# Kernel tuning notes

Hardware: AMD Instinct MI355X
Metric: run time of the kernel (lower is better)

The kernel has to match this reference:

```python
import jax, jax.numpy as jnp
import numpy as np

B, N, C, H = 16, 4096, 384, 8
D = C // H  # head_dim = 48
WSTD = 0.02


def setup_inputs() -> dict:
    key = jax.random.key(0)
    ks = jax.random.split(key, 9)
    return {
        "x": jax.random.normal(ks[0], (B, N, C), dtype=jnp.float32),
        "conv_w": jax.random.normal(ks[1], (C, C), dtype=jnp.float32) * WSTD,  # Conv1d k=1, squeezed
        "conv_b": jax.random.normal(ks[2], (C,), dtype=jnp.float32) * WSTD,
        "wq": jax.random.normal(ks[3], (C, C), dtype=jnp.float32) * WSTD,
        "bq": jax.random.normal(ks[4], (C,), dtype=jnp.float32) * WSTD,
        "wkv": jax.random.normal(ks[5], (2 * C, C), dtype=jnp.float32) * WSTD,
        "bkv": jax.random.normal(ks[6], (2 * C,), dtype=jnp.float32) * WSTD,
        "wp": jax.random.normal(ks[7], (C, C), dtype=jnp.float32) * WSTD,
        "bp": jax.random.normal(ks[8], (C,), dtype=jnp.float32) * WSTD,
    }


def reference(x, conv_w, conv_b, wq, bq, wkv, bkv, wp, bp):
    b, n, c = x.shape
    h, d = H, c // H
    # Conv1d kernel_size=1 over channels == per-token linear: y = x @ W^T + b
    x_in = jnp.einsum("bnc,oc->bno", x, conv_w) + conv_b  # [B,N,C]
    # q: reshape(B,N,1,H,d).permute(2,0,3,4,1)[0] -> [B,H,d,N]
    q = (x_in @ wq.T + bq).reshape(b, n, h, d).transpose(0, 2, 3, 1)  # [B,H,d,N]
    kv = (x_in @ wkv.T + bkv).reshape(b, n, 2, h, d).transpose(2, 0, 3, 4, 1)  # [2,B,H,d,N]
    k, v = kv[0], kv[1]
    scale = jnp.asarray(n, x.dtype) ** -0.5  # note: N^-0.5, not head_dim^-0.5
    attn = jax.nn.softmax((q * scale) @ jnp.swapaxes(k, -2, -1), axis=-1)  # [B,H,d,d]
    out = attn @ v  # [B,H,d,N]
    # transpose(1,2) -> [B,d,H,N], then raw reshape to [B,N,C] (verbatim torch layout)
    out = jnp.transpose(out, (0, 2, 1, 3)).reshape(b, n, c)
    return out @ wp.T + bp
```

## Files before the change

### kernel.cpp

```cpp
#include <hip/hip_runtime.h>
#include <hip/hip_bf16.h>
#include <stdint.h>

#define DEVI static __device__ __forceinline__

typedef __attribute__((ext_vector_type(4))) float f32x4;
typedef __attribute__((ext_vector_type(4))) unsigned int u32x4;
typedef __attribute__((ext_vector_type(8))) short bf16x8;
typedef unsigned short u16;
typedef unsigned int u32;
typedef unsigned long long u64;

#define BB 16
#define NN 4096
#define CC 384
#define HH 8
#define DD 48

DEVI u16 f2bf(float f) {
  union { float f; u32 u; } c; c.f = f;
  u32 u = c.u;
  u32 r = (u + 0x7FFFu + ((u >> 16) & 1u)) >> 16;
  return (u16)r;
}
DEVI float bf2f(u16 h) {
  union { float f; u32 u; } c; c.u = ((u32)h) << 16;
  return c.f;
}
DEVI void stage8(u16* dst, const float* src) {
  const f32x4 a = *(const f32x4*)(src);
  const f32x4 b = *(const f32x4*)(src + 4);
  union { bf16x8 v; u16 u[8]; } o;
  o.u[0] = f2bf(a[0]); o.u[1] = f2bf(a[1]); o.u[2] = f2bf(a[2]); o.u[3] = f2bf(a[3]);
  o.u[4] = f2bf(b[0]); o.u[5] = f2bf(b[1]); o.u[6] = f2bf(b[2]); o.u[7] = f2bf(b[3]);
  *(bf16x8*)dst = o.v;
}

typedef const __attribute__((address_space(1))) void* gas_ptr;
typedef __attribute__((address_space(3))) void* las_ptr;
DEVI void gload16(const void* g, void* l) {
  __builtin_amdgcn_global_load_lds((gas_ptr)g, (las_ptr)l, 16, 0, 0);
}

__global__ __launch_bounds__(256)
void f32_to_bf16(const float* __restrict__ in, u16* __restrict__ out, int n8) {
  const int i = blockIdx.x * 256 + threadIdx.x;
  if (i >= n8) return;
  u16 tmp[8];
  stage8(tmp, in + (size_t)i * 8);
  *(bf16x8*)(out + (size_t)i * 8) = *(bf16x8*)tmp;
}

__global__ __launch_bounds__(256)
void transpose_xb(const u16* __restrict__ xb, u16* __restrict__ xbT) {
  __shared__ u32 LtT[32 * 260];
  const int ct = blockIdx.x, nt = blockIdx.y, b = blockIdx.z;
  const int t = threadIdx.x;
  const int n0 = nt * 512, c0 = ct * 32;
  const int coct = t & 3, c = coct * 8;
  const int q = t >> 2;
  const int swzw = coct << 3;
#pragma unroll
  for (int p = 0; p < 4; ++p) {
    const int npair = q + p * 64;
    const int n = 2 * npair;
    const u16* s0 = &xb[((size_t)(b * NN + n0 + n)) * CC + c0 + c];
    union { bf16x8 v; u16 e[8]; } ua, ub;
    ua.v = *(const bf16x8*)s0;
    ub.v = *(const bf16x8*)(s0 + CC);
    const int npw = npair ^ swzw;
#pragma unroll
    for (int i = 0; i < 8; ++i)
      LtT[(c + i) * 260 + npw] = (u32)ua.e[i] | ((u32)ub.e[i] << 16);
  }
  __syncthreads();
#pragma unroll
  for (int p = 0; p < 8; ++p) {
    const int id = p * 256 + t;
    const int cc2 = id >> 6, ng = id & 63;
    const int swz2 = ((cc2 >> 3) & 3) << 3;
    union { u32x4 q4; bf16x8 o; } u;
    u.q4 = *(const u32x4*)&LtT[cc2 * 260 + ((ng * 4) ^ swz2)];
    *(bf16x8*)&xbT[((size_t)(b * CC + c0 + cc2)) * NN + n0 + ng * 8] = u.o;
  }
}

__global__ __launch_bounds__(256)
void prep_all(const float* __restrict__ wp, const float* __restrict__ wq,
              const float* __restrict__ wkv, const float* __restrict__ cw,
              const float* __restrict__ bq, const float* __restrict__ bkv,
              const float* __restrict__ cb, u16* __restrict__ wpb,
              u16* __restrict__ wtopb, u16* __restrict__ cwTb,
              float* __restrict__ bf_) {
  __shared__ u32 LtT[64 * 33];
  const int blk = blockIdx.x;
  const int t = threadIdx.x;
  if (blk < 288) {
    const float* src; u16* dst; int base;
    if (blk < 72)       { src = wp;  dst = wpb;             base = blk; }
    else if (blk < 144) { src = wq;  dst = wtopb;           base = blk - 72; }
    else                { src = wkv; dst = wtopb + CC * CC; base = blk - 144; }
    const int i = base * 256 + t;
    u16 tmp[8];
    stage8(tmp, src + (size_t)i * 8);
    *(bf16x8*)(dst + (size_t)i * 8) = *(bf16x8*)tmp;
  } else if (blk < 324) {
    const int blk2 = blk - 288;
    const int m0 = (blk2 / 6) * 64, c0 = (blk2 % 6) * 64;
    const int cl = (t & 15) * 4;
    const int mp = t >> 4;
#pragma unroll
    for (int pass = 0; pass < 2; ++pass) {
      const int w = mp + pass * 16;
      const int m = w * 2;
      const float* s0 = &cw[(size_t)(m0 + m) * CC + c0 + cl];
      const f32x4 a = *(const f32x4*)s0;
      const f32x4 bv = *(const f32x4*)(s0 + CC);
#pragma unroll
      for (int i = 0; i < 4; ++i)
        LtT[(cl + i) * 33 + w] = (u32)f2bf(a[i]) | ((u32)f2bf(bv[i]) << 16);
    }
    __syncthreads();
#pragma unroll
    for (int pass = 0; pass < 2; ++pass) {
      const int v = pass * 256 + t;
      const int c = v >> 3, mg = v & 7;
      union { bf16x8 o; u32 q[4]; } u;
#pragma unroll
      for (int r = 0; r < 4; ++r) u.q[r] = LtT[c * 33 + mg * 4 + r];
      *(bf16x8*)&cwTb[(size_t)(c0 + c) * CC + m0 + mg * 8] = u.o;
    }
  } else {
    const int o = (blk - 324) * 4 + (t >> 6);
    const int lane = t & 63;
    const float* wrow;
    float b0;
    if (o < CC) { wrow = wq + (size_t)o * CC;        b0 = bq[o]; }
    else        { wrow = wkv + (size_t)(o - CC) * CC; b0 = bkv[o - CC]; }
    float s = 0.f;
    for (int m = lane; m < CC; m += 64) s += wrow[m] * cb[m];
#pragma unroll
    for (int off = 32; off; off >>= 1) s += __shfl_xor(s, off, 64);
    if (lane == 0) bf_[o] = b0 + s;
  }
}

__global__ __launch_bounds__(256)
void colsum(const u16* __restrict__ xb, float* __restrict__ sx) {
  __shared__ float red[256][8];
  const int b = blockIdx.y, c0 = blockIdx.x * 64;
  const int t = threadIdx.x;
  const int c8 = t & 7, ns = t >> 3;
  const u16* src = xb + (size_t)b * NN * CC + c0 + c8 * 8;
  float a[8] = {};
  for (int it = 0; it < 128; ++it) {
    const bf16x8 v = *(const bf16x8*)(src + (size_t)(ns + 32 * it) * CC);
#pragma unroll
    for (int r = 0; r < 8; ++r) a[r] += bf2f((u16)v[r]);
  }
#pragma unroll
  for (int r = 0; r < 8; ++r) red[t][r] = a[r];
  __syncthreads();
  if (t < 64) {
    const int c8o = t >> 3, e = t & 7;
    float s = 0.f;
#pragma unroll
    for (int n2 = 0; n2 < 32; ++n2) s += red[c8o + 8 * n2][e];
    sx[b * CC + c0 + c8o * 8 + e] = s;
  }
}

__global__ __launch_bounds__(128)
void proj_sx(const u16* __restrict__ Wf, const float* __restrict__ sx,
             float* __restrict__ P) {
  __shared__ float sl[CC];
  const int b = blockIdx.y, o = blockIdx.x * 128 + threadIdx.x;
  for (int i = threadIdx.x; i < CC; i += 128) sl[i] = sx[b * CC + i];
  __syncthreads();
  float acc = 0.f;
  const u16* wr = Wf + (size_t)o * CC;
  for (int c8 = 0; c8 < CC; c8 += 8) {
    const bf16x8 w = *(const bf16x8*)(wr + c8);
#pragma unroll
    for (int r = 0; r < 8; ++r) acc += bf2f((u16)w[r]) * sl[c8 + r];
  }
  P[b * 768 + o] = acc;
}

template<typename OT, int BIASMODE, int TRI = 0, int SWZ = 1>
__global__ __launch_bounds__(512)
void gemm_f(const u16* __restrict__ A, const u16* __restrict__ W,
            const float* __restrict__ bias, OT* __restrict__ C,
            int M, int N, int K, int klen, int nbn, int nbm, int tpb,
            long sA, long sW, long sC, long sCp, long sBias) {
  constexpr int BK = 64;
  __shared__ __align__(16) u16 smem[32768];

  const int nx = gridDim.x;
  const int lin = blockIdx.x;
  const int lin2 = SWZ ? (lin & 7) * (nx >> 3) + (lin >> 3) : lin;
  const int b = lin2 / tpb;
  int t2 = lin2 % tpb;
  int bn, bm, p;
  if constexpr (TRI) {
    const int tl = t2 % 6; p = t2 / 6;
    bm = tl < 3 ? 0 : (tl < 5 ? 1 : 2);
    bn = tl < 3 ? tl : (tl < 5 ? tl - 2 : 2);
  } else {
    bn = t2 % nbn; t2 /= nbn;
    bm = t2 % nbm;
    p = t2 / nbm;
  }
  A += (size_t)b * sA; W += (size_t)b * sW;
  C += (size_t)b * sC + (size_t)p * sCp;
  if (BIASMODE) bias += (size_t)b * sBias;

  const int t = threadIdx.x;
  const int wid = t >> 6, lane = t & 63;
  const int wr = wid >> 2, wc = wid & 3;
  const int row0 = bm * 128, col0 = bn * 128;
  const int lrow = lane & 15;
  const int lswz = (lane & 7) << 3;
  const int kstart = p * klen;

  const int arow = t >> 3;
  const int scol = ((t & 7) ^ ((t >> 3) & 7)) * 8;
  const u16* Ag = A + (size_t)(row0 + arow) * K + scol;
  const u16* Wg = W + (size_t)(col0 + arow) * K + scol;

  f32x4 acc[4][2] = {};
  const int NT = klen >> 6;

  auto stage = [&](int buf, int kt) {
    u16* Al = smem + buf * 16384 + t * 8;
    u16* Bl = smem + buf * 16384 + 8192 + t * 8;
    const int k0 = kstart + kt * BK;
#pragma unroll
    for (int it = 0; it < 2; ++it) {
      gload16(Ag + (size_t)(it * 64) * K + k0, Al + it * 4096);
      gload16(Wg + (size_t)(it * 64) * K + k0, Bl + it * 4096);
    }
  };

  stage(0, 0);
  __syncthreads();
  int cur = 0;
  for (int kt = 0; kt < NT; ++kt) {
    if (kt + 1 < NT) stage(cur ^ 1, kt + 1);
    const u16* As = smem + cur * 16384;
    const u16* Bs = smem + cur * 16384 + 8192;
#pragma unroll
    for (int kk = 0; kk < 2; ++kk) {
      const int lk = (kk * 32 + (lane >> 4) * 8) ^ lswz;
      bf16x8 af[4], bfv[2];
#pragma unroll
      for (int i = 0; i < 4; ++i)
        af[i] = *(const bf16x8*)&As[(wr * 64 + i * 16 + lrow) * BK + lk];
#pragma unroll
      for (int j = 0; j < 2; ++j)
        bfv[j] = *(const bf16x8*)&Bs[(wc * 32 + j * 16 + lrow) * BK + lk];
#pragma unroll
      for (int i = 0; i < 4; ++i)
#pragma unroll
        for (int j = 0; j < 2; ++j)
          acc[i][j] = __builtin_amdgcn_mfma_f32_16x16x32_bf16(af[i], bfv[j], acc[i][j], 0, 0, 0);
    }
    __syncthreads();
    cur ^= 1;
  }

  const int lr = (lane >> 4) * 4;
  if constexpr (sizeof(OT) == 2) {
    u16* Ct = smem;
#pragma unroll
    for (int i = 0; i < 4; ++i)
#pragma unroll
      for (int j = 0; j < 2; ++j) {
        const int ccol = wc * 32 + j * 16 + lrow;
        float bv = 0.f;
        if constexpr (BIASMODE == 1) bv = bias[col0 + ccol];
#pragma unroll
        for (int r = 0; r < 4; ++r) {
          const int rrow = wr * 64 + i * 16 + lr + r;
          float b2 = bv;
          if constexpr (BIASMODE == 2) b2 = bias[row0 + rrow];
          Ct[rrow * 132 + ccol] = f2bf(acc[i][j][r] + b2);
        }
      }
    __syncthreads();
#pragma unroll
    for (int it = 0; it < 4; ++it) {
      const int id = it * 512 + t;
      const int row = id >> 4, c16 = (id & 15) * 8;
      *(bf16x8*)((u16*)C + (size_t)(row0 + row) * N + col0 + c16) =
          *(const bf16x8*)&Ct[row * 132 + c16];
    }
  } else {
    const int orow = row0 + wr * 64, ocol = col0 + wc * 32;
#pragma unroll
    for (int i = 0; i < 4; ++i)
#pragma unroll
      for (int j = 0; j < 2; ++j) {
        const int cc2 = ocol + j * 16 + lrow;
        float bv = 0.f;
        if constexpr (BIASMODE == 1) bv = bias[cc2];
#pragma unroll
        for (int r = 0; r < 4; ++r) {
          const int rr = orow + i * 16 + lr + r;
          float b2 = bv;
          if constexpr (BIASMODE == 2) b2 = bias[rr];
          C[(size_t)rr * N + cc2] = acc[i][j][r] + b2;
        }
      }
  }
}

__global__ __launch_bounds__(256)
void reduceG(const float* __restrict__ Gp, u16* __restrict__ Gbf) {
  __shared__ float lt[64 * 65];
  const int b = blockIdx.y;
  const int tile = blockIdx.x;
  const int ti = tile / 6, tj = tile % 6;
  const bool mir = (ti >> 1) > (tj >> 1);
  const int si = mir ? tj : ti, sj = mir ? ti : tj;
  const float* src = Gp + (size_t)b * 4 * 147456;
  u16* dst = Gbf + (size_t)b * 147456;
  const int t = threadIdx.x;
  const int r4 = t >> 4, c4 = (t & 15) * 4;
#pragma unroll
  for (int pass = 0; pass < 4; ++pass) {
    const int r = pass * 16 + r4;
    const size_t off = (size_t)(si * 64 + r) * CC + sj * 64 + c4;
    f32x4 s = *(const f32x4*)(src + off);
    s += *(const f32x4*)(src + 147456 + off);
    s += *(const f32x4*)(src + 2 * 147456 + off);
    s += *(const f32x4*)(src + 3 * 147456 + off);
    if (!mir) {
      union { u64 q; u16 e[4]; } o;
      o.e[0] = f2bf(s[0]); o.e[1] = f2bf(s[1]);
      o.e[2] = f2bf(s[2]); o.e[3] = f2bf(s[3]);
      *(u64*)&dst[(size_t)(ti * 64 + r) * CC + tj * 64 + c4] = o.q;
    } else {
#pragma unroll
      for (int k = 0; k < 4; ++k) lt[r * 65 + c4 + k] = s[k];
    }
  }
  if (mir) {
    __syncthreads();
#pragma unroll
    for (int pass = 0; pass < 4; ++pass) {
      const int i = pass * 16 + r4;
      union { u64 q; u16 e[4]; } o;
#pragma unroll
      for (int k = 0; k < 4; ++k) o.e[k] = f2bf(lt[(c4 + k) * 65 + i]);
      *(u64*)&dst[(size_t)(ti * 64 + i) * CC + tj * 64 + c4] = o.q;
    }
  }
}

__global__ __launch_bounds__(256)
void s_softmax(const u16* __restrict__ M1g, const u16* __restrict__ Wf,
               const float* __restrict__ bf_, const float* __restrict__ P,
               const u16* __restrict__ UvT, u16* __restrict__ AUb,
               float* __restrict__ rbias) {
  __shared__ float Sf[48 * 52];
  __shared__ __align__(16) u16 att[48 * 56];
  const int bh = blockIdx.x, b = bh >> 3, h = bh & 7;
  const int t = threadIdx.x, wid = t >> 6, lane = t & 63;
  const int lrow = lane & 15, lkq = lane >> 4;

  if (wid < 3) {
    f32x4 acc[3] = {};
    const u16* Arow = M1g + (size_t)b * 147456 + (size_t)(h * 48 + wid * 16 + lrow) * CC;
    const u16* Brow = Wf + (size_t)(CC + h * 48) * CC;
    for (int ks = 0; ks < 12; ++ks) {
      const int k = ks * 32 + lkq * 8;
      const bf16x8 af = *(const bf16x8*)(Arow + k);
#pragma unroll
      for (int j = 0; j < 3; ++j) {
        const bf16x8 bfr = *(const bf16x8*)(Brow + (size_t)(j * 16 + lrow) * CC + k);
        acc[j] = __builtin_amdgcn_mfma_f32_16x16x32_bf16(af, bfr, acc[j], 0, 0, 0);
      }
    }
    const int lr = lkq * 4;
#pragma unroll
    for (int j = 0; j < 3; ++j)
#pragma unroll
      for (int r = 0; r < 4; ++r)
        Sf[(wid * 16 + lr + r) * 52 + j * 16 + lrow] = acc[j][r];
  }
  __syncthreads();

  if (t < 48) {
    const float bi = bf_[h * 48 + t];
    const float pq = P[b * 768 + h * 48 + t];
    float row[48];
    float mx = -1e30f;
#pragma unroll
    for (int j = 0; j < 48; ++j) {
      const float g = bf_[CC + h * 48 + j];
      const float pk = P[b * 768 + CC + h * 48 + j];
      const float s = (Sf[t * 52 + j] + bi * pk + pq * g + 4096.f * bi * g) * 0.015625f;
      row[j] = s;
      mx = fmaxf(mx, s);
    }
    float sum = 0.f;
#pragma unroll
    for (int j = 0; j < 48; ++j) { row[j] = __expf(row[j] - mx); sum += row[j]; }
    const float inv = 1.f / sum;
    float rb = 0.f;
#pragma unroll
    for (int j = 0; j < 48; ++j) {
      const float a = row[j] * inv;
      att[t * 56 + j] = f2bf(a);
      rb += a * bf_[2 * CC + h * 48 + j];
    }
#pragma unroll
    for (int j = 48; j < 56; ++j) att[t * 56 + j] = 0;
    rbias[b * CC + t * 8 + h] = rb;
  }
  __syncthreads();

  f32x4 acc[3][6] = {};
  const u16* Vbase = UvT + h * 48;
  const bf16x8 z = {};
#pragma unroll
  for (int kk = 0; kk < 2; ++kk) {
    const int k = kk * 32 + lkq * 8;
    bf16x8 af[3];
#pragma unroll
    for (int i = 0; i < 3; ++i) {
      af[i] = *(const bf16x8*)&att[(i * 16 + lrow) * 56 + k];
      if (k >= 48) af[i] = z;
    }
#pragma unroll
    for (int ct = 0; ct < 6; ++ct) {
      const int c = wid * 96 + ct * 16 + lrow;
      bf16x8 bfr = *(const bf16x8*)(Vbase + (size_t)c * CC + k);
      if (k >= 48) bfr = z;
#pragma unroll
      for (int i = 0; i < 3; ++i)
        acc[i][ct] = __builtin_amdgcn_mfma_f32_16x16x32_bf16(af[i], bfr, acc[i][ct], 0, 0, 0);
    }
  }
  const int lr = lkq * 4;
#pragma unroll
  for (int i = 0; i < 3; ++i)
#pragma unroll
    for (int ct = 0; ct < 6; ++ct) {
      const int c = wid * 96 + ct * 16 + lrow;
#pragma unroll
      for (int r = 0; r < 4; ++r) {
        const int ii = i * 16 + lr + r;
        AUb[(size_t)b * 147456 + (size_t)(ii * 8 + h) * CC + c] = f2bf(acc[i][ct][r]);
      }
    }
}

extern "C" void kernel_launch(void* const* d_in, const int* in_sizes, int n_in,
                              void* d_out, int out_size, void* d_ws, size_t ws_size,
                              hipStream_t stream) {
  const float* x      = (const float*)d_in[0];
  const float* conv_w = (const float*)d_in[1];
  const float* conv_b = (const float*)d_in[2];
  const float* wq     = (const float*)d_in[3];
  const float* bq     = (const float*)d_in[4];
  const float* wkv    = (const float*)d_in[5];
  const float* bkv    = (const float*)d_in[6];
  const float* wp     = (const float*)d_in[7];
  const float* bp     = (const float*)d_in[8];
  float* y = (float*)d_out;

  char* ws = (char*)d_ws;
  u16*   Wf    = (u16*)(ws + 0);
  float* bf_   = (float*)(ws + 884736);
  u16*   wpb   = (u16*)(ws + 889344);
  u16*   UvT   = (u16*)(ws + 1184256);
  float* sx    = (float*)(ws + 1479168);
  float* P     = (float*)(ws + 1503744);
  float* rb    = (float*)(ws + 1552896);
  u16*   M1g   = (u16*)(ws + 1577472);
  u16*   Gbf   = (u16*)(ws + 6296064);
  u16*   AUb   = (u16*)(ws + 11014656);
  float* Gpart = (float*)(ws + 15733248);
  u16*   wtopb = (u16*)(ws + 53481984);
  u16*   cwTb  = (u16*)(ws + 54366720);
  u16*   xb    = (u16*)(ws + 54661632);
  u16*   xbT   = (u16*)(ws + 104993280);
  u16*   R     = xbT;

  f32_to_bf16<<<dim3((BB * NN * CC) / 8 / 256), dim3(256), 0, stream>>>(
      x, xb, (BB * NN * CC) / 8);
  transpose_xb<<<dim3(12, 8, 16), dim3(256), 0, stream>>>(xb, xbT);
  prep_all<<<dim3(612), dim3(256), 0, stream>>>(wp, wq, wkv, conv_w, bq, bkv,
                                                conv_b, wpb, wtopb, cwTb, bf_);
  gemm_f<u16, 0, 0, 0><<<dim3(18), dim3(512), 0, stream>>>(
      wtopb, cwTb, nullptr, Wf, 2 * CC, CC, CC, CC, 3, 6, 18,
      0, 0, 0, 0, 0);
  gemm_f<u16, 0, 0, 0><<<dim3(9), dim3(512), 0, stream>>>(
      cwTb, wtopb + 2 * CC * CC, nullptr, UvT, CC, CC, CC, CC, 3, 3, 9,
      0, 0, 0, 0, 0);
  colsum<<<dim3(6, 16), dim3(256), 0, stream>>>(xb, sx);
  proj_sx<<<dim3(6, 16), dim3(128), 0, stream>>>(Wf, sx, P);
  gemm_f<float, 0, 1><<<dim3(384), dim3(512), 0, stream>>>(
      xbT, xbT, nullptr, Gpart, CC, CC, NN, 1024, 3, 3, 24,
      (long)CC * NN, (long)CC * NN, 4L * 147456, 147456, 0);
  reduceG<<<dim3(36, 16), dim3(256), 0, stream>>>(Gpart, Gbf);
  gemm_f<u16, 0><<<dim3(144), dim3(512), 0, stream>>>(
      Wf, Gbf, nullptr, M1g, CC, CC, CC, CC, 3, 3, 9,
      0, 147456, 147456, 0, 0);
  s_softmax<<<dim3(128), dim3(256), 0, stream>>>(M1g, Wf, bf_, P, UvT, AUb, rb);
  gemm_f<u16, 2><<<dim3(1536), dim3(512), 0, stream>>>(
      AUb, xb, rb, R, CC, NN, CC, CC, 32, 3, 96,
      147456, (long)NN * CC, (long)NN * CC, 0, CC);
  gemm_f<float, 1><<<dim3(1536), dim3(512), 0, stream>>>(
      R, wpb, bp, y, BB * NN, CC, CC, CC, 3, 512, 1536,
      0, 0, 0, 0, 0);
}
```

Measured before the change: 214.5 us.

## Merge prep kernels: fuse cast with weight prep, transpose with colsum, dual small GEMMs

The f32->bf16 cast of x now runs in the same launch as the weight preparation, with four vectors per thread. The transpose and a split column-sum (four partial slices over N) share one launch, and proj_sx adds up the partials. The two small weight-product GEMMs run as a single dual-problem launch. This cuts launch count and serialization gaps between small kernels and gives colsum more parallelism. In exchange it adds branching inside kernels and reuses the Gpart buffer as scratch for the partial sums.

```diff
diff --git a/kernel.cpp b/kernel.cpp
--- a/kernel.cpp
+++ b/kernel.cpp
@@ -43,58 +43,27 @@
 }
 
 __global__ __launch_bounds__(256)
-void f32_to_bf16(const float* __restrict__ in, u16* __restrict__ out, int n8) {
-  const int i = blockIdx.x * 256 + threadIdx.x;
-  if (i >= n8) return;
-  u16 tmp[8];
-  stage8(tmp, in + (size_t)i * 8);
-  *(bf16x8*)(out + (size_t)i * 8) = *(bf16x8*)tmp;
-}
-
-__global__ __launch_bounds__(256)
-void transpose_xb(const u16* __restrict__ xb, u16* __restrict__ xbT) {
-  __shared__ u32 LtT[32 * 260];
-  const int ct = blockIdx.x, nt = blockIdx.y, b = blockIdx.z;
+void conv_fused(const float* __restrict__ x, u16* __restrict__ xb,
+                const float* __restrict__ wp, const float* __restrict__ wq,
+                const float* __restrict__ wkv, const float* __restrict__ cw,
+                const float* __restrict__ bq, const float* __restrict__ bkv,
+                const float* __restrict__ cb, u16* __restrict__ wpb,
+                u16* __restrict__ wtopb, u16* __restrict__ cwTb,
+                float* __restrict__ bf_) {
+  __shared__ u32 LtT[64 * 33];
+  const int bid = blockIdx.x;
   const int t = threadIdx.x;
-  const int n0 = nt * 512, c0 = ct * 32;
-  const int coct = t & 3, c = coct * 8;
-  const int q = t >> 2;
-  const int swzw = coct << 3;
-#pragma unroll
-  for (int p = 0; p < 4; ++p) {
-    const int npair = q + p * 64;
-    const int n = 2 * npair;
-    const u16* s0 = &xb[((size_t)(b * NN + n0 + n)) * CC + c0 + c];
-    union { bf16x8 v; u16 e[8]; } ua, ub;
-    ua.v = *(const bf16x8*)s0;
-    ub.v = *(const bf16x8*)(s0 + CC);
-    const int npw = npair ^ swzw;
-#pragma unroll
-    for (int i = 0; i < 8; ++i)
-      LtT[(c + i) * 260 + npw] = (u32)ua.e[i] | ((u32)ub.e[i] << 16);
-  }
-  __syncthreads();
-#pragma unroll
-  for (int p = 0; p < 8; ++p) {
-    const int id = p * 256 + t;
-    const int cc2 = id >> 6, ng = id & 63;
-    const int swz2 = ((cc2 >> 3) & 3) << 3;
-    union { u32x4 q4; bf16x8 o; } u;
-    u.q4 = *(const u32x4*)&LtT[cc2 * 260 + ((ng * 4) ^ swz2)];
-    *(bf16x8*)&xbT[((size_t)(b * CC + c0 + cc2)) * NN + n0 + ng * 8] = u.o;
-  }
-}
-
-__global__ __launch_bounds__(256)
-void prep_all(const float* __restrict__ wp, const float* __restrict__ wq,
-              const float* __restrict__ wkv, const float* __restrict__ cw,
-              const float* __restrict__ bq, const float* __restrict__ bkv,
-              const float* __restrict__ cb, u16* __restrict__ wpb,
-              u16* __restrict__ wtopb, u16* __restrict__ cwTb,
-              float* __restrict__ bf_) {
-  __shared__ u32 LtT[64 * 33];
-  const int blk = blockIdx.x;
-  const int t = threadIdx.x;
+  if (bid < 3072) {
+#pragma unroll
+    for (int pass = 0; pass < 4; ++pass) {
+      const size_t i = ((size_t)(bid * 4 + pass) * 256 + t) * 8;
+      u16 tmp[8];
+      stage8(tmp, x + i);
+      *(bf16x8*)(xb + i) = *(bf16x8*)tmp;
+    }
+    return;
+  }
+  const int blk = bid - 3072;
   if (blk < 288) {
     const float* src; u16* dst; int base;
     if (blk < 72)       { src = wp;  dst = wpb;             base = blk; }
@@ -146,36 +115,76 @@
 }
 
 __global__ __launch_bounds__(256)
-void colsum(const u16* __restrict__ xb, float* __restrict__ sx) {
-  __shared__ float red[256][8];
-  const int b = blockIdx.y, c0 = blockIdx.x * 64;
+void trans_colsum(const u16* __restrict__ xb, u16* __restrict__ xbT,
+                  float* __restrict__ sxp) {
+  __shared__ __align__(16) char smem[33280];
+  const int bid = blockIdx.x;
   const int t = threadIdx.x;
-  const int c8 = t & 7, ns = t >> 3;
-  const u16* src = xb + (size_t)b * NN * CC + c0 + c8 * 8;
-  float a[8] = {};
-  for (int it = 0; it < 128; ++it) {
-    const bf16x8 v = *(const bf16x8*)(src + (size_t)(ns + 32 * it) * CC);
-#pragma unroll
-    for (int r = 0; r < 8; ++r) a[r] += bf2f((u16)v[r]);
-  }
-#pragma unroll
-  for (int r = 0; r < 8; ++r) red[t][r] = a[r];
-  __syncthreads();
-  if (t < 64) {
-    const int c8o = t >> 3, e = t & 7;
-    float s = 0.f;
-#pragma unroll
-    for (int n2 = 0; n2 < 32; ++n2) s += red[c8o + 8 * n2][e];
-    sx[b * CC + c0 + c8o * 8 + e] = s;
+  if (bid < 1536) {
+    u32* LtT = (u32*)smem;
+    const int ct = bid % 12, nt = (bid / 12) % 8, b = bid / 96;
+    const int n0 = nt * 512, c0 = ct * 32;
+    const int coct = t & 3, c = coct * 8;
+    const int q = t >> 2;
+    const int swzw = coct << 3;
+#pragma unroll
+    for (int p = 0; p < 4; ++p) {
+      const int npair = q + p * 64;
+      const int n = 2 * npair;
+      const u16* s0 = &xb[((size_t)(b * NN + n0 + n)) * CC + c0 + c];
+      union { bf16x8 v; u16 e[8]; } ua, ub;
+      ua.v = *(const bf16x8*)s0;
+      ub.v = *(const bf16x8*)(s0 + CC);
+      const int npw = npair ^ swzw;
+#pragma unroll
+      for (int i = 0; i < 8; ++i)
+        LtT[(c + i) * 260 + npw] = (u32)ua.e[i] | ((u32)ub.e[i] << 16);
+    }
+    __syncthreads();
+#pragma unroll
+    for (int p = 0; p < 8; ++p) {
+      const int id = p * 256 + t;
+      const int cc2 = id >> 6, ng = id & 63;
+      const int swz2 = ((cc2 >> 3) & 3) << 3;
+      union { u32x4 q4; bf16x8 o; } u;
+      u.q4 = *(const u32x4*)&LtT[cc2 * 260 + ((ng * 4) ^ swz2)];
+      *(bf16x8*)&xbT[((size_t)(b * CC + c0 + cc2)) * NN + n0 + ng * 8] = u.o;
+    }
+  } else {
+    float (*red)[8] = (float(*)[8])smem;
+    const int k = bid - 1536;
+    const int p = k & 3, k2 = k >> 2;
+    const int c0 = (k2 % 6) * 64, b = k2 / 6;
+    const int c8 = t & 7, ns = t >> 3;
+    const u16* src = xb + (size_t)b * NN * CC + (size_t)(p * 1024) * CC +
+                     c0 + c8 * 8;
+    float a[8] = {};
+    for (int it = 0; it < 32; ++it) {
+      const bf16x8 v = *(const bf16x8*)(src + (size_t)(ns + 32 * it) * CC);
+#pragma unroll
+      for (int r = 0; r < 8; ++r) a[r] += bf2f((u16)v[r]);
+    }
+#pragma unroll
+    for (int r = 0; r < 8; ++r) red[t][r] = a[r];
+    __syncthreads();
+    if (t < 64) {
+      const int c8o = t >> 3, e = t & 7;
+      float s = 0.f;
+#pragma unroll
+      for (int n2 = 0; n2 < 32; ++n2) s += red[c8o + 8 * n2][e];
+      sxp[(size_t)(p * 16 + b) * CC + c0 + c8o * 8 + e] = s;
+    }
   }
 }
 
 __global__ __launch_bounds__(128)
-void proj_sx(const u16* __restrict__ Wf, const float* __restrict__ sx,
+void proj_sx(const u16* __restrict__ Wf, const float* __restrict__ sxp,
              float* __restrict__ P) {
   __shared__ float sl[CC];
   const int b = blockIdx.y, o = blockIdx.x * 128 + threadIdx.x;
-  for (int i = threadIdx.x; i < CC; i += 128) sl[i] = sx[b * CC + i];
+  for (int i = threadIdx.x; i < CC; i += 128)
+    sl[i] = sxp[(size_t)b * CC + i] + sxp[(size_t)(16 + b) * CC + i] +
+            sxp[(size_t)(32 + b) * CC + i] + sxp[(size_t)(48 + b) * CC + i];
   __syncthreads();
   float acc = 0.f;
   const u16* wr = Wf + (size_t)o * CC;
@@ -187,29 +196,37 @@
   P[b * 768 + o] = acc;
 }
 
-template<typename OT, int BIASMODE, int TRI = 0, int SWZ = 1>
+template<typename OT, int BIASMODE, int TRI = 0, int SWZ = 1, int DUAL = 0>
 __global__ __launch_bounds__(512)
 void gemm_f(const u16* __restrict__ A, const u16* __restrict__ W,
             const float* __restrict__ bias, OT* __restrict__ C,
             int M, int N, int K, int klen, int nbn, int nbm, int tpb,
-            long sA, long sW, long sC, long sCp, long sBias) {
+            long sA, long sW, long sC, long sCp, long sBias,
+            const u16* __restrict__ A2, const u16* __restrict__ W2,
+            OT* __restrict__ C2) {
   constexpr int BK = 64;
   __shared__ __align__(16) u16 smem[32768];
 
   const int nx = gridDim.x;
   const int lin = blockIdx.x;
   const int lin2 = SWZ ? (lin & 7) * (nx >> 3) + (lin >> 3) : lin;
-  const int b = lin2 / tpb;
-  int t2 = lin2 % tpb;
-  int bn, bm, p;
-  if constexpr (TRI) {
-    const int tl = t2 % 6; p = t2 / 6;
-    bm = tl < 3 ? 0 : (tl < 5 ? 1 : 2);
-    bn = tl < 3 ? tl : (tl < 5 ? tl - 2 : 2);
+  int b, bn, bm, p;
+  if constexpr (DUAL) {
+    int l = lin2;
+    if (l >= 18) { A = A2; W = W2; C = C2; l -= 18; }
+    bn = l % 3; bm = l / 3; p = 0; b = 0;
   } else {
-    bn = t2 % nbn; t2 /= nbn;
-    bm = t2 % nbm;
-    p = t2 / nbm;
+    b = lin2 / tpb;
+    int t2 = lin2 % tpb;
+    if constexpr (TRI) {
+      const int tl = t2 % 6; p = t2 / 6;
+      bm = tl < 3 ? 0 : (tl < 5 ? 1 : 2);
+      bn = tl < 3 ? tl : (tl < 5 ? tl - 2 : 2);
+    } else {
+      bn = t2 % nbn; t2 /= nbn;
+      bm = t2 % nbm;
+      p = t2 / nbm;
+    }
   }
   A += (size_t)b * sA; W += (size_t)b * sW;
   C += (size_t)b * sC + (size_t)p * sCp;
@@ -476,44 +493,39 @@
   float* bf_   = (float*)(ws + 884736);
   u16*   wpb   = (u16*)(ws + 889344);
   u16*   UvT   = (u16*)(ws + 1184256);
-  float* sx    = (float*)(ws + 1479168);
   float* P     = (float*)(ws + 1503744);
   float* rb    = (float*)(ws + 1552896);
   u16*   M1g   = (u16*)(ws + 1577472);
   u16*   Gbf   = (u16*)(ws + 6296064);
   u16*   AUb   = (u16*)(ws + 11014656);
   float* Gpart = (float*)(ws + 15733248);
+  float* sxp   = Gpart;
   u16*   wtopb = (u16*)(ws + 53481984);
   u16*   cwTb  = (u16*)(ws + 54366720);
   u16*   xb    = (u16*)(ws + 54661632);
   u16*   xbT   = (u16*)(ws + 104993280);
   u16*   R     = xbT;
 
-  f32_to_bf16<<<dim3((BB * NN * CC) / 8 / 256), dim3(256), 0, stream>>>(
-      x, xb, (BB * NN * CC) / 8);
-  transpose_xb<<<dim3(12, 8, 16), dim3(256), 0, stream>>>(xb, xbT);
-  prep_all<<<dim3(612), dim3(256), 0, stream>>>(wp, wq, wkv, conv_w, bq, bkv,
-                                                conv_b, wpb, wtopb, cwTb, bf_);
-  gemm_f<u16, 0, 0, 0><<<dim3(18), dim3(512), 0, stream>>>(
-      wtopb, cwTb, nullptr, Wf, 2 * CC, CC, CC, CC, 3, 6, 18,
-      0, 0, 0, 0, 0);
-  gemm_f<u16, 0, 0, 0><<<dim3(9), dim3(512), 0, stream>>>(
-      cwTb, wtopb + 2 * CC * CC, nullptr, UvT, CC, CC, CC, CC, 3, 3, 9,
-      0, 0, 0, 0, 0);
-  colsum<<<dim3(6, 16), dim3(256), 0, stream>>>(xb, sx);
-  proj_sx<<<dim3(6, 16), dim3(128), 0, stream>>>(Wf, sx, P);
+  conv_fused<<<dim3(3684), dim3(256), 0, stream>>>(
+      x, xb, wp, wq, wkv, conv_w, bq, bkv, conv_b, wpb, wtopb, cwTb, bf_);
+  trans_colsum<<<dim3(1920), dim3(256), 0, stream>>>(xb, xbT, sxp);
+  gemm_f<u16, 0, 0, 0, 1><<<dim3(27), dim3(512), 0, stream>>>(
+      wtopb, cwTb, nullptr, Wf, 2 * CC, CC, CC, CC, 3, 6, 27,
+      0, 0, 0, 0, 0, cwTb, wtopb + 2 * CC * CC, UvT);
+  proj_sx<<<dim3(6, 16), dim3(128), 0, stream>>>(Wf, sxp, P);
   gemm_f<float, 0, 1><<<dim3(384), dim3(512), 0, stream>>>(
       xbT, xbT, nullptr, Gpart, CC, CC, NN, 1024, 3, 3, 24,
-      (long)CC * NN, (long)CC * NN, 4L * 147456, 147456, 0);
+      (long)CC * NN, (long)CC * NN, 4L * 147456, 147456, 0,
+      nullptr, nullptr, nullptr);
   reduceG<<<dim3(36, 16), dim3(256), 0, stream>>>(Gpart, Gbf);
   gemm_f<u16, 0><<<dim3(144), dim3(512), 0, stream>>>(
       Wf, Gbf, nullptr, M1g, CC, CC, CC, CC, 3, 3, 9,
-      0, 147456, 147456, 0, 0);
+      0, 147456, 147456, 0, 0, nullptr, nullptr, nullptr);
   s_softmax<<<dim3(128), dim3(256), 0, stream>>>(M1g, Wf, bf_, P, UvT, AUb, rb);
   gemm_f<u16, 2><<<dim3(1536), dim3(512), 0, stream>>>(
       AUb, xb, rb, R, CC, NN, CC, CC, 32, 3, 96,
-      147456, (long)NN * CC, (long)NN * CC, 0, CC);
+      147456, (long)NN * CC, (long)NN * CC, 0, CC, nullptr, nullptr, nullptr);
   gemm_f<float, 1><<<dim3(1536), dim3(512), 0, stream>>>(
       R, wpb, bp, y, BB * NN, CC, CC, CC, 3, 512, 1536,
-      0, 0, 0, 0, 0);
-}
+      0, 0, 0, 0, 0, nullptr, nullptr, nullptr);
+}
```

Result: faster. 201.2 us (-6.2%).
